# Kernel tuning notes

Measured on AMD Instinct MI355X. Metric: run time of the kernel, lower is better.

Reference implementation:

```python
import jax, jax.numpy as jnp
import numpy as np

B, L, D, H = 1, 2048, 3072, 24
Dh = D // H            # 128
MLP = 4 * D            # 12288
EPS = 1e-6


def setup_inputs() -> dict:
    key = jax.random.key(0)
    ks = jax.random.split(key, 10)
    n = lambda k, shape, s=1.0: jax.random.normal(k, shape, jnp.float32) * s
    W = 0.02  # weight init scale
    return {
        "img": n(ks[0], (B, L, D)),
        "vec": n(ks[1], (B, D)),
        "pe": n(ks[2], (1, 1, L, Dh // 2, 2, 2)),
        "mod_w": n(ks[3], (D, 3 * D), W),
        "mod_b": jnp.zeros((3 * D,), jnp.float32),
        "lin1_w": n(ks[4], (D, 3 * D + MLP), W),
        "lin1_b": jnp.zeros((3 * D + MLP,), jnp.float32),
        "lin2_w": n(ks[5], (D + MLP, D), W),
        "lin2_b": jnp.zeros((D,), jnp.float32),
        "q_scale": jnp.ones((Dh,), jnp.float32),
        "k_scale": jnp.ones((Dh,), jnp.float32),
    }


def _rms_norm(x, scale):
    return x * jax.lax.rsqrt(jnp.mean(x * x, axis=-1, keepdims=True) + EPS) * scale


def _apply_rope(x, pe):
    # x: [B,H,L,Dh]; pe: [1,1,L,Dh/2,2,2]
    xr = x.reshape(*x.shape[:-1], Dh // 2, 1, 2)
    out = pe[..., 0] * xr[..., 0] + pe[..., 1] * xr[..., 1]  # [B,H,L,Dh/2,2]
    return out.reshape(*x.shape[:-1], Dh)


def reference(img, vec, pe, mod_w, mod_b, lin1_w, lin1_b, lin2_w, lin2_b, q_scale, k_scale):
    # adaLN modulation (single): shift / scale / gate, each [B,1,D]
    mod = jax.nn.silu(vec) @ mod_w + mod_b
    shift, scale, gate = jnp.split(mod[:, None, :], 3, axis=-1)

    # pre-norm LayerNorm (no affine) + modulation
    mu = jnp.mean(img, axis=-1, keepdims=True)
    var = jnp.var(img, axis=-1, keepdims=True)
    x = (1.0 + scale) * ((img - mu) * jax.lax.rsqrt(var + EPS)) + shift

    # fused QKV + MLP projection
    proj = x @ lin1_w + lin1_b                     # [B,L,3D+MLP]
    qkv, mlp = proj[..., : 3 * D], proj[..., 3 * D :]

    # 'B L (K H D) -> K B H L D'
    qkv = qkv.reshape(B, L, 3, H, Dh).transpose(2, 0, 3, 1, 4)
    q, k, v = qkv[0], qkv[1], qkv[2]

    # per-head QK RMSNorm
    q = _rms_norm(q, q_scale)
    k = _rms_norm(k, k_scale)

    # RoPE
    q = _apply_rope(q, pe)
    k = _apply_rope(k, pe)

    # attention (scale = head_dim**-0.5)
    scores = jnp.einsum("bhqd,bhkd->bhqk", q, k) * (Dh ** -0.5)
    probs = jax.nn.softmax(scores, axis=-1)
    attn = jnp.einsum("bhqk,bhkd->bhqd", probs, v)
    attn = attn.transpose(0, 2, 1, 3).reshape(B, L, D)  # 'B H L D -> B L (H D)'

    # gated parallel MLP output + residual
    out = jnp.concatenate([attn, jax.nn.gelu(mlp, approximate=True)], axis=-1) @ lin2_w + lin2_b
    return img + gate * out
```

## Files before the change

kernel.cpp:

```cpp
#include <hip/hip_runtime.h>
#include <hip/hip_bf16.h>
#include <stdint.h>


#define DEV static __device__ __forceinline__

typedef __attribute__((ext_vector_type(4))) float f32x4;
typedef __attribute__((ext_vector_type(16))) float f32x16;
typedef __attribute__((ext_vector_type(8))) short s8v;

DEV unsigned short f2bf(float f) {
  union { float f; unsigned u; } v; v.f = f;
  unsigned r = v.u + 0x7fffu + ((v.u >> 16) & 1u);
  return (unsigned short)(r >> 16);
}
DEV float bf2f(unsigned short b) {
  union { unsigned u; float f; } v; v.u = ((unsigned)b) << 16; return v.f;
}
DEV unsigned pk2bf(float a, float b) {
  union { __hip_bfloat162 h; unsigned u; } v;
  v.h = __float22bfloat162_rn(make_float2(a, b));
  return v.u;
}

DEV void gl_lds16(const void* g, void* l) {
  __builtin_amdgcn_global_load_lds(
      (const __attribute__((address_space(1))) unsigned int*)(uintptr_t)g,
      (__attribute__((address_space(3))) unsigned int*)(uint32_t)(uintptr_t)l,
      16, 0, 0);
}

__global__ __launch_bounds__(256) void modvec_partial(
    const float* __restrict__ vec, const float* __restrict__ mod_w, float* __restrict__ part) {
  __shared__ float s[384];
  const int tid = threadIdx.x;
  const int i0 = blockIdx.y * 384;
  for (int i = tid; i < 384; i += 256) {
    float v = vec[i0 + i];
    s[i] = v / (1.f + __expf(-v));
  }
  __syncthreads();
  const int j = blockIdx.x * 256 + tid;
  float acc = 0.f;
#pragma unroll 8
  for (int i = 0; i < 384; ++i) acc += s[i] * mod_w[(size_t)(i0 + i) * 9216 + j];
  part[(size_t)blockIdx.y * 9216 + j] = acc;
}

__global__ __launch_bounds__(256) void modvec_reduce(
    const float* __restrict__ part, const float* __restrict__ mod_b, float* __restrict__ mod) {
  const int j = blockIdx.x * 256 + threadIdx.x;
  float a = mod_b[j];
#pragma unroll
  for (int y = 0; y < 8; ++y) a += part[(size_t)y * 9216 + j];
  mod[j] = a;
}

__global__ __launch_bounds__(256) void ln_mod_kernel(
    const float* __restrict__ img, const float* __restrict__ mod, unsigned short* __restrict__ x) {
  const int l = blockIdx.x, tid = threadIdx.x;
  const int wave = tid >> 6;
  const f32x4* row = (const f32x4*)(img + (size_t)l * 3072);
  f32x4 v[3];
  float s = 0.f, s2 = 0.f;
#pragma unroll
  for (int i = 0; i < 3; ++i) {
    v[i] = row[tid + i * 256];
#pragma unroll
    for (int c = 0; c < 4; ++c) { s += v[i][c]; s2 += v[i][c] * v[i][c]; }
  }
#pragma unroll
  for (int m = 1; m < 64; m <<= 1) { s += __shfl_xor(s, m); s2 += __shfl_xor(s2, m); }
  __shared__ float rs[4], rs2[4];
  if ((tid & 63) == 0) { rs[wave] = s; rs2[wave] = s2; }
  __syncthreads();
  s = rs[0] + rs[1] + rs[2] + rs[3];
  s2 = rs2[0] + rs2[1] + rs2[2] + rs2[3];
  const float mu = s * (1.f / 3072.f);
  const float var = s2 * (1.f / 3072.f) - mu * mu;
  const float inv = rsqrtf(var + 1e-6f);
#pragma unroll
  for (int i = 0; i < 3; ++i) {
    int d0 = (tid + i * 256) * 4;
    unsigned out[2];
    unsigned short o[4];
#pragma unroll
    for (int c = 0; c < 4; ++c) {
      int d = d0 + c;
      float val = (1.f + mod[3072 + d]) * ((v[i][c] - mu) * inv) + mod[d];
      o[c] = f2bf(val);
    }
    out[0] = o[0] | ((unsigned)o[1] << 16);
    out[1] = o[2] | ((unsigned)o[3] << 16);
    *(uint2*)(x + (size_t)l * 3072 + d0) = make_uint2(out[0], out[1]);
  }
}

__global__ __launch_bounds__(256) void transpose_kernel(
    const float* __restrict__ W, unsigned short* __restrict__ Wt, int K, int N) {
  __shared__ float t[64][65];
  const int k0 = blockIdx.x * 64, n0 = blockIdx.y * 64;
  const int tid = threadIdx.x;
#pragma unroll
  for (int it = 0; it < 4; ++it) {
    const int k = it * 16 + (tid >> 4), c4 = (tid & 15) * 4;
    f32x4 v = *(const f32x4*)&W[(size_t)(k0 + k) * N + n0 + c4];
    t[k][c4] = v[0]; t[k][c4 + 1] = v[1]; t[k][c4 + 2] = v[2]; t[k][c4 + 3] = v[3];
  }
  __syncthreads();
#pragma unroll
  for (int it = 0; it < 2; ++it) {
    const int idx = it * 256 + tid;
    const int n = idx >> 3, k8 = (idx & 7) * 8;
    s8v o;
#pragma unroll
    for (int e = 0; e < 8; ++e) o[e] = (short)f2bf(t[k8 + e][n]);
    *(s8v*)&Wt[(size_t)(n0 + n) * K + k0 + k8] = o;
  }
}

template <int EPI>
__global__ __launch_bounds__(512, 2) void gemm256_kernel(
    const unsigned short* __restrict__ A, const unsigned short* __restrict__ Bt,
    const float* __restrict__ bias, void* __restrict__ Cout, void* __restrict__ Cout2,
    int K, int N, int nTile, int nBN) {
  __shared__ unsigned short lds[65536];
  const int tid = threadIdx.x;
  const int lane = tid & 63, w = tid >> 6;
  const int wm = w >> 2, wn = w & 3;
  const int l15 = lane & 15, l4 = lane >> 4;

  int bid = blockIdx.x;
  const int nwg = gridDim.x;
  bid = (bid & 7) * (nwg >> 3) + (bid >> 3);
  const int bz = bid / (nBN << 3);
  const int rem = bid - bz * (nBN << 3);
  const int m0 = (rem & 7) << 8;
  const int n0 = (rem >> 3) << 8;
  const int kOff = bz * nTile * 64;

  const int sr = (w << 3) + (lane >> 3);
  const int skc = ((lane & 7) ^ (sr & 7)) << 3;
  const size_t aBase = (size_t)m0 * K + kOff;
  const size_t bBase = (size_t)n0 * K + kOff;

  const int xs0 = (l4 ^ (l15 & 7)) << 3;
  const int xs1 = ((4 + l4) ^ (l15 & 7)) << 3;
  int aRow[4], bRow[2];
#pragma unroll
  for (int i = 0; i < 4; ++i) aRow[i] = (wm * 64 + i * 16 + l15) * 64;
#pragma unroll
  for (int j = 0; j < 2; ++j) bRow[j] = (wn * 32 + j * 16 + l15) * 64;

  f32x4 acc[2][2][4][2];
#pragma unroll
  for (int mq = 0; mq < 2; ++mq)
#pragma unroll
    for (int nq = 0; nq < 2; ++nq)
#pragma unroll
      for (int i = 0; i < 4; ++i)
#pragma unroll
        for (int j = 0; j < 2; ++j) acc[mq][nq][i][j] = (f32x4){0.f, 0.f, 0.f, 0.f};

#define STAGE(op, h, par, kt)                                                        \
  do {                                                                               \
    const unsigned short* _s = (op) ? Bt : A;                                        \
    const size_t _b = (op) ? bBase : aBase;                                          \
    unsigned short* _d = &lds[((par) << 15) + ((op) << 14) + ((h) << 13) + (w << 9)];\
    gl_lds16(_s + _b + (size_t)((h) * 128 + sr) * K + (kt) * 64 + skc, _d);          \
    gl_lds16(_s + _b + (size_t)((h) * 128 + 64 + sr) * K + (kt) * 64 + skc, _d + 4096);\
  } while (0)

#define FRAGP(op, h, rowoff, xsv) \
  (*(const s8v*)&lds[pB + ((op) << 14) + ((h) << 13) + (rowoff) + (xsv)])

#define PH_MID()                                            \
  __builtin_amdgcn_s_barrier();                             \
  asm volatile("s_waitcnt lgkmcnt(0)" ::: "memory");        \
  __builtin_amdgcn_sched_barrier(0);                        \
  __builtin_amdgcn_s_setprio(1)

#define PH_END()                                            \
  __builtin_amdgcn_s_setprio(0);                            \
  __builtin_amdgcn_s_barrier()

#define PH_END_VM()                                         \
  __builtin_amdgcn_s_setprio(0);                            \
  asm volatile("s_waitcnt vmcnt(6)" ::: "memory");          \
  __builtin_amdgcn_s_barrier()

#define MFMA_QUAD(mq, nq)                                                              \
  _Pragma("unroll") for (int i = 0; i < 4; ++i) _Pragma("unroll") for (int j = 0; j < 2; ++j) { \
    acc[mq][nq][i][j] =                                                                \
        __builtin_amdgcn_mfma_f32_16x16x32_bf16(a[i][0], b[nq][j][0], acc[mq][nq][i][j], 0, 0, 0); \
    acc[mq][nq][i][j] =                                                                \
        __builtin_amdgcn_mfma_f32_16x16x32_bf16(a[i][1], b[nq][j][1], acc[mq][nq][i][j], 0, 0, 0); \
  }

  STAGE(0, 0, 0, 0); STAGE(1, 0, 0, 0); STAGE(1, 1, 0, 0); STAGE(0, 1, 0, 0);
  {
    const int k1 = (nTile > 1) ? 1 : 0;
    STAGE(0, 0, 1, k1); STAGE(1, 0, 1, k1); STAGE(1, 1, 1, k1);
  }
  asm volatile("s_waitcnt vmcnt(6)" ::: "memory");
  __builtin_amdgcn_s_barrier();

  s8v a[4][2], b[2][2][2];
#pragma unroll 2
  for (int t = 0; t < nTile; ++t) {
    const int pB = (t & 1) << 15;
    const int kt1 = (t + 1 < nTile) ? t + 1 : 0;
    const int kt2 = (t + 2 < nTile) ? t + 2 : 0;
#pragma unroll
    for (int i = 0; i < 4; ++i) { a[i][0] = FRAGP(0, 0, aRow[i], xs0); a[i][1] = FRAGP(0, 0, aRow[i], xs1); }
#pragma unroll
    for (int j = 0; j < 2; ++j) { b[0][j][0] = FRAGP(1, 0, bRow[j], xs0); b[0][j][1] = FRAGP(1, 0, bRow[j], xs1); }
    STAGE(0, 1, (t + 1) & 1, kt1);
    PH_MID();
    MFMA_QUAD(0, 0);
    PH_END();
#pragma unroll
    for (int j = 0; j < 2; ++j) { b[1][j][0] = FRAGP(1, 1, bRow[j], xs0); b[1][j][1] = FRAGP(1, 1, bRow[j], xs1); }
    STAGE(0, 0, t & 1, kt2);
    PH_MID();
    MFMA_QUAD(0, 1);
    PH_END();
#pragma unroll
    for (int i = 0; i < 4; ++i) { a[i][0] = FRAGP(0, 1, aRow[i], xs0); a[i][1] = FRAGP(0, 1, aRow[i], xs1); }
    STAGE(1, 0, t & 1, kt2);
    PH_MID();
    MFMA_QUAD(1, 0);
    PH_END();
    STAGE(1, 1, t & 1, kt2);
    PH_MID();
    MFMA_QUAD(1, 1);
    PH_END_VM();
  }

  asm volatile("s_waitcnt vmcnt(0)" ::: "memory");
  __builtin_amdgcn_s_barrier();

  if (EPI == 0) {
    if (n0 < 9216) {
#pragma unroll
      for (int mq = 0; mq < 2; ++mq)
#pragma unroll
        for (int nq = 0; nq < 2; ++nq)
#pragma unroll
          for (int j = 0; j < 2; ++j) {
            const int col = n0 + nq * 128 + wn * 32 + j * 16 + l15;
            const float bj = bias[col];
#pragma unroll
            for (int i = 0; i < 4; ++i) {
              const int row0 = m0 + mq * 128 + wm * 64 + i * 16 + (l4 << 2);
#pragma unroll
              for (int r = 0; r < 4; ++r)
                ((unsigned short*)Cout)[(size_t)(row0 + r) * 9216 + col] =
                    f2bf(acc[mq][nq][i][j][r] + bj);
            }
          }
    } else {
#pragma unroll
      for (int mq = 0; mq < 2; ++mq)
#pragma unroll
        for (int nq = 0; nq < 2; ++nq)
#pragma unroll
          for (int j = 0; j < 2; ++j) {
            const int col = n0 + nq * 128 + wn * 32 + j * 16 + l15;
            const float bj = bias[col];
#pragma unroll
            for (int i = 0; i < 4; ++i) {
              const int row0 = m0 + mq * 128 + wm * 64 + i * 16 + (l4 << 2);
#pragma unroll
              for (int r = 0; r < 4; ++r) {
                const float v = acc[mq][nq][i][j][r] + bj;
                const float y = 0.7978845608f * (v + 0.044715f * v * v * v);
                const float ex = exp2f(2.8853900818f * y);
                const float g = v - v * __builtin_amdgcn_rcpf(ex + 1.f);
                ((unsigned short*)Cout2)[(size_t)(row0 + r) * 15360 + (col - 6144)] = f2bf(g);
              }
            }
          }
    }
  } else {
#pragma unroll
    for (int mq = 0; mq < 2; ++mq)
#pragma unroll
      for (int nq = 0; nq < 2; ++nq)
#pragma unroll
        for (int j = 0; j < 2; ++j) {
          const int col = n0 + nq * 128 + wn * 32 + j * 16 + l15;
#pragma unroll
          for (int i = 0; i < 4; ++i) {
            const int row0 = m0 + mq * 128 + wm * 64 + i * 16 + (l4 << 2);
#pragma unroll
            for (int r = 0; r < 4; ++r)
              ((float*)Cout)[(size_t)bz * 2048 * N + (size_t)(row0 + r) * N + col] =
                  acc[mq][nq][i][j][r];
          }
        }
  }
#undef STAGE
#undef FRAGP
#undef PH_MID
#undef PH_END
#undef PH_END_VM
#undef MFMA_QUAD
}

__global__ __launch_bounds__(256) void reduce2_kernel(
    const float* __restrict__ part, const float* __restrict__ img,
    const float* __restrict__ mod, const float* __restrict__ bias, float* __restrict__ out) {
  const size_t idx = ((size_t)blockIdx.x * 256 + threadIdx.x) * 4;
  const int col = (int)(idx % 3072);
  f32x4 p0 = *(const f32x4*)(part + idx);
  f32x4 p1 = *(const f32x4*)(part + (size_t)6291456 + idx);
  f32x4 p2 = *(const f32x4*)(part + 2 * (size_t)6291456 + idx);
  f32x4 p3 = *(const f32x4*)(part + 3 * (size_t)6291456 + idx);
  f32x4 p4 = *(const f32x4*)(part + 4 * (size_t)6291456 + idx);
  f32x4 im = *(const f32x4*)(img + idx);
  f32x4 o;
#pragma unroll
  for (int e = 0; e < 4; ++e)
    o[e] = im[e] +
           mod[6144 + col + e] * (((p0[e] + p1[e]) + (p2[e] + p3[e])) + p4[e] + bias[col + e]);
  *(f32x4*)(out + idx) = o;
}

DEV void qk_one(const unsigned short* src, const float* sc, const f32x4 pe4, float extra,
                unsigned short* dst, int lane) {
  unsigned xx = *(const unsigned*)(src + 2 * lane);
  float x0 = bf2f((unsigned short)(xx & 0xffff));
  float x1 = bf2f((unsigned short)(xx >> 16));
  float ss = x0 * x0 + x1 * x1;
#pragma unroll
  for (int m = 1; m < 64; m <<= 1) ss += __shfl_xor(ss, m);
  const float inv = rsqrtf(ss * (1.f / 128.f) + 1e-6f);
  x0 *= inv * sc[2 * lane];
  x1 *= inv * sc[2 * lane + 1];
  float o0 = (pe4.x * x0 + pe4.y * x1) * extra;
  float o1 = (pe4.z * x0 + pe4.w * x1) * extra;
  *(unsigned*)(dst + 2 * lane) = (unsigned)f2bf(o0) | ((unsigned)f2bf(o1) << 16);
}

__global__ __launch_bounds__(256) void qk_prep_kernel(
    const unsigned short* __restrict__ proj, const float* __restrict__ pe,
    const float* __restrict__ q_scale, const float* __restrict__ k_scale,
    unsigned short* __restrict__ qr, unsigned short* __restrict__ kr) {
  const int l = blockIdx.x;
  const int tid = threadIdx.x, lane = tid & 63, wave = tid >> 6;
  const unsigned short* row = proj + (size_t)l * 9216;
  const f32x4 pe4 = *(const f32x4*)(pe + ((size_t)l * 64 + lane) * 4);
  const float qsc = 0.12751743761f;
#pragma unroll
  for (int hh = 0; hh < 6; ++hh) {
    const int h = wave + hh * 4;
    qk_one(row + h * 128, q_scale, pe4, qsc, qr + ((size_t)h * 2048 + l) * 128, lane);
    qk_one(row + 3072 + h * 128, k_scale, pe4, 1.f, kr + ((size_t)h * 2048 + l) * 128, lane);
  }
}

__global__ __launch_bounds__(256) void vtrans_kernel(
    const unsigned short* __restrict__ proj, unsigned short* __restrict__ vt) {
  __shared__ unsigned short t[128][136];
  const int h = blockIdx.y, l0 = blockIdx.x * 128;
  const int tid = threadIdx.x;
  const int row = tid >> 1, half = tid & 1;
  const unsigned short* src = proj + (size_t)(l0 + row) * 9216 + 6144 + h * 128 + half * 64;
#pragma unroll
  for (int cc = 0; cc < 8; ++cc)
    *(s8v*)&t[row][half * 64 + cc * 8] = *(const s8v*)(src + cc * 8);
  __syncthreads();
  const int dh = tid >> 1;
  unsigned short* dst = vt + ((size_t)h * 128 + dh) * 2048 + l0 + half * 64;
#pragma unroll
  for (int lc = 0; lc < 8; ++lc) {
    s8v o;
#pragma unroll
    for (int e = 0; e < 8; ++e) o[e] = (short)t[half * 64 + lc * 8 + e][dh];
    *(s8v*)(dst + lc * 8) = o;
  }
}

__global__ __launch_bounds__(256) void attn_kernel(
    const unsigned short* __restrict__ qr, const unsigned short* __restrict__ kr,
    const unsigned short* __restrict__ vt, unsigned short* __restrict__ A2) {
  __shared__ char lds[65536];
  const int tid = threadIdx.x, lane = tid & 63, w = tid >> 6;
  const int l31 = lane & 31, hi = lane >> 5;
  const int h = blockIdx.y;
  const int q0 = blockIdx.x * 128 + w * 32;
  const int q = q0 + l31;

  s8v qf[8];
  {
    const unsigned short* qb = qr + ((size_t)h * 2048 + q) * 128 + hi * 8;
#pragma unroll
    for (int ks = 0; ks < 8; ++ks) qf[ks] = *(const s8v*)(qb + ks * 16);
  }

  int koff[4], voff[4];
#pragma unroll
  for (int c = 0; c < 4; ++c) {
    const int ob = (w * 4 + c) * 1024 + lane * 16;
    const int row = ob >> 8;
    const int sl = (ob >> 4) & 15;
    const int ssl = sl ^ (row & 15);
    koff[c] = row * 128 + ssl * 8;
    const int dh = row * 2 + (ssl >> 3);
    voff[c] = dh * 2048 + (ssl & 7) * 8;
  }
  const unsigned short* krH = kr + (size_t)h * 2048 * 128;
  const unsigned short* vtH = vt + (size_t)h * 128 * 2048;

  f32x16 oacc[4];
#pragma unroll
  for (int rf = 0; rf < 4; ++rf)
#pragma unroll
    for (int e = 0; e < 16; ++e) oacc[rf][e] = 0.f;
  float m = -3e38f, l = 0.f;

#define ATT_STAGE(t)                                                        \
  do {                                                                      \
    char* kb_ = lds + ((t) & 1) * 32768;                                    \
    char* vb_ = kb_ + 16384;                                                \
    _Pragma("unroll") for (int c = 0; c < 4; ++c) {                         \
      gl_lds16(krH + (size_t)(t) * 8192 + koff[c], kb_ + (w * 4 + c) * 1024); \
      gl_lds16(vtH + (size_t)(t) * 64 + voff[c], vb_ + (w * 4 + c) * 1024);   \
    }                                                                       \
  } while (0)

  ATT_STAGE(0);
  __syncthreads();

  for (int t = 0; t < 32; ++t) {
    if (t + 1 < 32) ATT_STAGE(t + 1);
    char* kb = lds + (t & 1) * 32768;
    char* vb = kb + 16384;

    f32x16 st[2];
#pragma unroll
    for (int rf = 0; rf < 2; ++rf)
#pragma unroll
      for (int e = 0; e < 16; ++e) st[rf][e] = 0.f;
#pragma unroll
    for (int ks = 0; ks < 8; ++ks)
#pragma unroll
      for (int rf = 0; rf < 2; ++rf) {
        const int kvr = rf * 32 + l31;
        s8v kf = *(const s8v*)(kb + kvr * 256 + (((ks * 2 + hi) ^ (kvr & 15)) << 4));
        st[rf] = __builtin_amdgcn_mfma_f32_32x32x16_bf16(kf, qf[ks], st[rf], 0, 0, 0);
      }

    float pm = st[0][0];
#pragma unroll
    for (int rf = 0; rf < 2; ++rf)
#pragma unroll
      for (int e = 0; e < 16; ++e) pm = fmaxf(pm, st[rf][e]);
    pm = fmaxf(pm, __shfl_xor(pm, 32));
    if (__any(pm - m > 11.5f)) {
      const float mn = fmaxf(m, pm);
      const float rs = exp2f(m - mn);
      l *= rs;
#pragma unroll
      for (int rf = 0; rf < 4; ++rf)
#pragma unroll
        for (int e = 0; e < 16; ++e) oacc[rf][e] *= rs;
      m = mn;
    }
    unsigned P2[16];
#pragma unroll
    for (int rb = 0; rb < 2; ++rb)
#pragma unroll
      for (int g = 0; g < 4; ++g) {
        const float e0 = exp2f(st[rb][4 * g + 0] - m);
        const float e1 = exp2f(st[rb][4 * g + 1] - m);
        const float e2 = exp2f(st[rb][4 * g + 2] - m);
        const float e3 = exp2f(st[rb][4 * g + 3] - m);
        l += (e0 + e1) + (e2 + e3);
        P2[rb * 8 + g * 2 + 0] = pk2bf(e0, e1);
        P2[rb * 8 + g * 2 + 1] = pk2bf(e2, e3);
      }

#pragma unroll
    for (int ks = 0; ks < 4; ++ks) {
      const int iA = ((2 * ks) >> 2) * 8 + ((2 * ks) & 3) * 2;
      const int iB = ((2 * ks + 1) >> 2) * 8 + ((2 * ks + 1) & 3) * 2;
      const unsigned s0 = hi ? P2[iA] : P2[iB];
      const unsigned s1 = hi ? P2[iA + 1] : P2[iB + 1];
      const unsigned r0 = (unsigned)__shfl_xor((int)s0, 32);
      const unsigned r1 = (unsigned)__shfl_xor((int)s1, 32);
      const unsigned o0 = hi ? P2[iB] : P2[iA];
      const unsigned o1 = hi ? P2[iB + 1] : P2[iA + 1];
      union { unsigned u[4]; s8v v; } pf;
      pf.u[0] = hi ? r0 : o0;
      pf.u[1] = hi ? r1 : o1;
      pf.u[2] = hi ? o0 : r0;
      pf.u[3] = hi ? o1 : r1;
#pragma unroll
      for (int rf = 0; rf < 4; ++rf) {
        const int dh = rf * 32 + l31, r = dh >> 1;
        const int sl = ((dh & 1) << 3) + ks * 2 + hi;
        s8v vf = *(const s8v*)(vb + r * 256 + ((sl ^ (r & 15)) << 4));
        oacc[rf] = __builtin_amdgcn_mfma_f32_32x32x16_bf16(vf, pf.v, oacc[rf], 0, 0, 0);
      }
    }
    __syncthreads();
  }

  const float lf = l + __shfl_xor(l, 32);
  const float inv = 1.f / lf;
  char* ep = lds + w * 8448;
#pragma unroll
  for (int rf = 0; rf < 4; ++rf)
#pragma unroll
    for (int g = 0; g < 4; ++g) {
      const unsigned u0 = pk2bf(oacc[rf][4 * g + 0] * inv, oacc[rf][4 * g + 1] * inv);
      const unsigned u1 = pk2bf(oacc[rf][4 * g + 2] * inv, oacc[rf][4 * g + 3] * inv);
      *(uint2*)(ep + l31 * 264 + rf * 64 + g * 16 + hi * 8) = make_uint2(u0, u1);
    }
  __syncthreads();
  const int c = lane & 15, l4b = lane >> 4;
#pragma unroll
  for (int pass = 0; pass < 8; ++pass) {
    const int qq = pass * 4 + l4b;
    const uint2 a2 = *(const uint2*)(ep + qq * 264 + c * 16);
    const uint2 b2 = *(const uint2*)(ep + qq * 264 + c * 16 + 8);
    *(uint4*)(A2 + (size_t)(q0 + qq) * 15360 + h * 128 + c * 8) =
        make_uint4(a2.x, a2.y, b2.x, b2.y);
  }
#undef ATT_STAGE
}

extern "C" void kernel_launch(void* const* d_in, const int* in_sizes, int n_in,
                              void* d_out, int out_size, void* d_ws, size_t ws_size,
                              hipStream_t stream) {
  (void)in_sizes; (void)n_in; (void)out_size; (void)ws_size;
  const float* img    = (const float*)d_in[0];
  const float* vec    = (const float*)d_in[1];
  const float* pe     = (const float*)d_in[2];
  const float* mod_w  = (const float*)d_in[3];
  const float* mod_b  = (const float*)d_in[4];
  const float* lin1_w = (const float*)d_in[5];
  const float* lin1_b = (const float*)d_in[6];
  const float* lin2_w = (const float*)d_in[7];
  const float* lin2_b = (const float*)d_in[8];
  const float* q_s    = (const float*)d_in[9];
  const float* k_s    = (const float*)d_in[10];
  float* out = (float*)d_out;

  char* ws = (char*)d_ws;
  size_t off = 0;
  auto alloc = [&](size_t b) { size_t p = off; off += (b + 255) & ~(size_t)255; return p; };
  float* part          = (float*)(ws + alloc((size_t)8 * 9216 * 4));
  float* mod           = (float*)(ws + alloc((size_t)9216 * 4));
  unsigned short* x    = (unsigned short*)(ws + alloc((size_t)2048 * 3072 * 2));
  unsigned short* wT   = (unsigned short*)(ws + alloc((size_t)21504 * 3072 * 2));
  unsigned short* proj = (unsigned short*)(ws + alloc((size_t)2048 * 21504 * 2));
  unsigned short* qr   = (unsigned short*)(ws + alloc((size_t)24 * 2048 * 128 * 2));
  unsigned short* kr   = (unsigned short*)(ws + alloc((size_t)24 * 2048 * 128 * 2));
  unsigned short* vt   = (unsigned short*)(ws + alloc((size_t)24 * 128 * 2048 * 2));
  unsigned short* A2   = (unsigned short*)(ws + alloc((size_t)2048 * 15360 * 2));
  float* p2buf = (float*)proj;

  modvec_partial<<<dim3(36, 8), 256, 0, stream>>>(vec, mod_w, part);
  modvec_reduce<<<36, 256, 0, stream>>>(part, mod_b, mod);
  ln_mod_kernel<<<2048, 256, 0, stream>>>(img, mod, x);
  transpose_kernel<<<dim3(48, 336), 256, 0, stream>>>(lin1_w, wT, 3072, 21504);
  gemm256_kernel<0><<<672, 512, 0, stream>>>(x, wT, lin1_b, proj, A2, 3072, 21504, 48, 84);
  qk_prep_kernel<<<2048, 256, 0, stream>>>(proj, pe, q_s, k_s, qr, kr);
  vtrans_kernel<<<dim3(16, 24), 256, 0, stream>>>(proj, vt);
  attn_kernel<<<dim3(16, 24), 256, 0, stream>>>(qr, kr, vt, A2);
  transpose_kernel<<<dim3(240, 48), 256, 0, stream>>>(lin2_w, wT, 15360, 3072);
  gemm256_kernel<2><<<480, 512, 0, stream>>>(A2, wT, nullptr, p2buf, nullptr, 15360, 3072, 48, 12);
  reduce2_kernel<<<6144, 256, 0, stream>>>(p2buf, img, mod, lin2_b, out);
}
```

Measured before the change: 845.6 us.

## Double-buffer LDS fragment registers to overlap ds_reads with MFMA phases

Restructures the GEMM main loop so each phase's LDS fragment reads for the next quadrant are issued inside the current MFMA phase, using separate A/B register buffers (aA/aB, b0/b1). Fragments for the next k-tile are prefetched from the other LDS parity before the loop wraps, and vmcnt waits are tightened per phase so the prefetched tile has landed. This hides LDS read latency behind matrix instructions at the cost of more VGPRs and tighter synchronisation correctness requirements.

```diff
diff --git a/kernel.cpp b/kernel.cpp
--- a/kernel.cpp
+++ b/kernel.cpp
@@ -171,30 +171,44 @@
     gl_lds16(_s + _b + (size_t)((h) * 128 + 64 + sr) * K + (kt) * 64 + skc, _d + 4096);\
   } while (0)
 
-#define FRAGP(op, h, rowoff, xsv) \
-  (*(const s8v*)&lds[pB + ((op) << 14) + ((h) << 13) + (rowoff) + (xsv)])
-
-#define PH_MID()                                            \
+#define FRAGP(op, h, par, rowoff, xsv) \
+  (*(const s8v*)&lds[((par) << 15) + ((op) << 14) + ((h) << 13) + (rowoff) + (xsv)])
+
+#define RD_A(dst, h, par)                                                       \
+  _Pragma("unroll") for (int i = 0; i < 4; ++i) {                               \
+    dst[i][0] = FRAGP(0, h, par, aRow[i], xs0);                                 \
+    dst[i][1] = FRAGP(0, h, par, aRow[i], xs1);                                 \
+  }
+
+#define RD_B(dst, h, par)                                                       \
+  _Pragma("unroll") for (int j = 0; j < 2; ++j) {                               \
+    dst[j][0] = FRAGP(1, h, par, bRow[j], xs0);                                 \
+    dst[j][1] = FRAGP(1, h, par, bRow[j], xs1);                                 \
+  }
+
+#define PH_OPEN()                                           \
   __builtin_amdgcn_s_barrier();                             \
   asm volatile("s_waitcnt lgkmcnt(0)" ::: "memory");        \
   __builtin_amdgcn_sched_barrier(0);                        \
   __builtin_amdgcn_s_setprio(1)
 
-#define PH_END()                                            \
+#define PH_CLOSE()                                          \
+  __builtin_amdgcn_sched_barrier(0);                        \
   __builtin_amdgcn_s_setprio(0);                            \
   __builtin_amdgcn_s_barrier()
 
-#define PH_END_VM()                                         \
+#define PH_CLOSE_VM(NN)                                     \
+  __builtin_amdgcn_sched_barrier(0);                        \
   __builtin_amdgcn_s_setprio(0);                            \
-  asm volatile("s_waitcnt vmcnt(6)" ::: "memory");          \
+  asm volatile("s_waitcnt vmcnt(" #NN ")" ::: "memory");    \
   __builtin_amdgcn_s_barrier()
 
-#define MFMA_QUAD(mq, nq)                                                              \
+#define MFMA_QUAD(mq, nq, av, bv)                                                      \
   _Pragma("unroll") for (int i = 0; i < 4; ++i) _Pragma("unroll") for (int j = 0; j < 2; ++j) { \
     acc[mq][nq][i][j] =                                                                \
-        __builtin_amdgcn_mfma_f32_16x16x32_bf16(a[i][0], b[nq][j][0], acc[mq][nq][i][j], 0, 0, 0); \
+        __builtin_amdgcn_mfma_f32_16x16x32_bf16(av[i][0], bv[j][0], acc[mq][nq][i][j], 0, 0, 0); \
     acc[mq][nq][i][j] =                                                                \
-        __builtin_amdgcn_mfma_f32_16x16x32_bf16(a[i][1], b[nq][j][1], acc[mq][nq][i][j], 0, 0, 0); \
+        __builtin_amdgcn_mfma_f32_16x16x32_bf16(av[i][1], bv[j][1], acc[mq][nq][i][j], 0, 0, 0); \
   }
 
   STAGE(0, 0, 0, 0); STAGE(1, 0, 0, 0); STAGE(1, 1, 0, 0); STAGE(0, 1, 0, 0);
@@ -205,39 +219,38 @@
   asm volatile("s_waitcnt vmcnt(6)" ::: "memory");
   __builtin_amdgcn_s_barrier();
 
-  s8v a[4][2], b[2][2][2];
+  s8v aA[4][2], aB[4][2], b0[2][2], b1[2][2];
+  RD_A(aA, 0, 0);
+  RD_B(b0, 0, 0);
+
 #pragma unroll 2
   for (int t = 0; t < nTile; ++t) {
-    const int pB = (t & 1) << 15;
+    const int p = t & 1, pn = p ^ 1;
     const int kt1 = (t + 1 < nTile) ? t + 1 : 0;
     const int kt2 = (t + 2 < nTile) ? t + 2 : 0;
-#pragma unroll
-    for (int i = 0; i < 4; ++i) { a[i][0] = FRAGP(0, 0, aRow[i], xs0); a[i][1] = FRAGP(0, 0, aRow[i], xs1); }
-#pragma unroll
-    for (int j = 0; j < 2; ++j) { b[0][j][0] = FRAGP(1, 0, bRow[j], xs0); b[0][j][1] = FRAGP(1, 0, bRow[j], xs1); }
-    STAGE(0, 1, (t + 1) & 1, kt1);
-    PH_MID();
-    MFMA_QUAD(0, 0);
-    PH_END();
-#pragma unroll
-    for (int j = 0; j < 2; ++j) { b[1][j][0] = FRAGP(1, 1, bRow[j], xs0); b[1][j][1] = FRAGP(1, 1, bRow[j], xs1); }
-    STAGE(0, 0, t & 1, kt2);
-    PH_MID();
-    MFMA_QUAD(0, 1);
-    PH_END();
-#pragma unroll
-    for (int i = 0; i < 4; ++i) { a[i][0] = FRAGP(0, 1, aRow[i], xs0); a[i][1] = FRAGP(0, 1, aRow[i], xs1); }
-    STAGE(1, 0, t & 1, kt2);
-    PH_MID();
-    MFMA_QUAD(1, 0);
-    PH_END();
-    STAGE(1, 1, t & 1, kt2);
-    PH_MID();
-    MFMA_QUAD(1, 1);
-    PH_END_VM();
-  }
-
-  asm volatile("s_waitcnt vmcnt(0)" ::: "memory");
+    STAGE(0, 1, pn, kt1);
+    PH_OPEN();
+    RD_B(b1, 1, p);
+    MFMA_QUAD(0, 0, aA, b0);
+    PH_CLOSE();
+    STAGE(0, 0, p, kt2);
+    PH_OPEN();
+    RD_A(aB, 1, p);
+    MFMA_QUAD(0, 1, aA, b1);
+    PH_CLOSE_VM(8);
+    STAGE(1, 0, p, kt2);
+    PH_OPEN();
+    RD_A(aA, 0, pn);
+    MFMA_QUAD(1, 0, aB, b0);
+    PH_CLOSE_VM(8);
+    STAGE(1, 1, p, kt2);
+    PH_OPEN();
+    RD_B(b0, 0, pn);
+    MFMA_QUAD(1, 1, aB, b1);
+    PH_CLOSE_VM(6);
+  }
+
+  asm volatile("s_waitcnt vmcnt(0) lgkmcnt(0)" ::: "memory");
   __builtin_amdgcn_s_barrier();
 
   if (EPI == 0) {
@@ -302,9 +315,11 @@
   }
 #undef STAGE
 #undef FRAGP
-#undef PH_MID
-#undef PH_END
-#undef PH_END_VM
+#undef RD_A
+#undef RD_B
+#undef PH_OPEN
+#undef PH_CLOSE
+#undef PH_CLOSE_VM
 #undef MFMA_QUAD
 }
 
```

Result: no change. 840.5 us (-0.6%).
